# Kernel tuning notes

Hardware: AMD Instinct MI355X
Metric: run time of the kernel (lower is better)

## Reference

```python
import jax, jax.numpy as jnp
import numpy as np

B, N, D, H = 2, 2048, 384, 8
Dh = D // H          # 48
G = Dh // 3          # 16 3-vectors per head
EPS = 1e-5


def setup_inputs() -> dict:
    key = jax.random.key(0)
    ks = jax.random.split(key, 8)
    x = jax.random.normal(ks[0], (B, N, D), dtype=jnp.float32)
    # per-node SE(3) frames: proper rotation matrices via QR of random Gaussians
    raw = jax.random.normal(ks[1], (B, N, 3, 3), dtype=jnp.float32)
    q, r = jnp.linalg.qr(raw)
    sign = jnp.sign(jnp.diagonal(r, axis1=-2, axis2=-1))
    frames = q * sign[..., None, :]
    s = 1.0 / np.sqrt(D)
    Wq = jax.random.normal(ks[2], (D, D), dtype=jnp.float32) * s
    Wk = jax.random.normal(ks[3], (D, D), dtype=jnp.float32) * s
    Wv = jax.random.normal(ks[4], (D, D), dtype=jnp.float32) * s
    Wo = jax.random.normal(ks[5], (D, D), dtype=jnp.float32) * s
    bo = jnp.zeros((D,), dtype=jnp.float32)
    gamma = jnp.ones((D,), dtype=jnp.float32)
    beta = jnp.zeros((D,), dtype=jnp.float32)
    return {"x": x, "frames": frames, "Wq": Wq, "Wk": Wk, "Wv": Wv,
            "Wo": Wo, "bo": bo, "gamma": gamma, "beta": beta}


def _rotate(frames, t):
    # t: [B,N,H,Dh] -> rotate each 3-vector chunk by the node's frame R_i
    b, n, h, dh = t.shape
    t3 = t.reshape(b, n, h, dh // 3, 3)
    r3 = jnp.einsum('bnij,bnhgj->bnhgi', frames, t3)
    return r3.reshape(b, n, h, dh)


def reference(x, frames, Wq, Wk, Wv, Wo, bo, gamma, beta):
    b, n, d = x.shape
    Q = (x @ Wq.T).reshape(b, n, H, Dh)
    K = (x @ Wk.T).reshape(b, n, H, Dh)
    V = (x @ Wv.T).reshape(b, n, H, Dh)
    # SE(3) frame-conditioned attention: rotate Q,K into each node's local frame
    Qr = _rotate(frames, Q)
    Kr = _rotate(frames, K)
    scores = jnp.einsum('bqhd,bkhd->bhqk', Qr, Kr) / np.sqrt(Dh)
    attn = jax.nn.softmax(scores, axis=-1)
    out = jnp.einsum('bhqk,bkhd->bqhd', attn, V).reshape(b, n, d)
    out = out @ Wo.T + bo          # out_proj; dropout is identity in eval
    y = x + out                     # residual
    mu = jnp.mean(y, axis=-1, keepdims=True)
    var = jnp.var(y, axis=-1, keepdims=True)
    return (y - mu) * jax.lax.rsqrt(var + EPS) * gamma + beta
```

## Files before the change

kernel.cpp:

```cpp
#include <hip/hip_runtime.h>
#include <hip/hip_bf16.h>
#include <math.h>

constexpr int B = 2, N = 2048, D = 384, H = 8, Dh = 48;
constexpr int M = B * N;
constexpr float EPS = 1e-5f;
constexpr int WSZ = 384 * 384;

typedef short bf16x8 __attribute__((ext_vector_type(8)));
typedef float f32x4 __attribute__((ext_vector_type(4)));

#if __has_builtin(__builtin_amdgcn_exp2f)
#define EXP2(x) __builtin_amdgcn_exp2f(x)
#else
#define EXP2(x) exp2f(x)
#endif

__device__ __forceinline__ ushort f2bf(float f) {
  union { float f; uint u; } v; v.f = f;
  uint r = v.u + 0x7fffu + ((v.u >> 16) & 1u);
  return (ushort)(r >> 16);
}
__device__ __forceinline__ float bf2f(ushort u) {
  union { uint u; float f; } v; v.u = ((uint)u) << 16;
  return v.f;
}
__device__ __forceinline__ uint pk_bf16(float lo, float hi) {
  union { __hip_bfloat162 h; uint u; } v;
  v.h = __float22bfloat162_rn(make_float2(lo, hi));
  return v.u;
}

__device__ __forceinline__ void gload16(const void* g, void* lds) {
  __builtin_amdgcn_global_load_lds(
      (const __attribute__((address_space(1))) unsigned int*)g,
      (__attribute__((address_space(3))) unsigned int*)lds, 16, 0, 0);
}

__global__ __launch_bounds__(256) void pack_all(
    const float* __restrict__ x, const float* __restrict__ Wq,
    const float* __restrict__ Wk, const float* __restrict__ Wv,
    const float* __restrict__ Wo, ushort* __restrict__ xbf,
    ushort* __restrict__ Wqkv, ushort* __restrict__ Wobf) {
  constexpr int XSZ = M * 384;
  int i = (blockIdx.x * 256 + threadIdx.x) * 8;
  const float* src; ushort* dst; int off;
  if (i < XSZ) { src = x; dst = xbf; off = i; }
  else {
    int j = i - XSZ;
    if (j < WSZ)          { src = Wq; dst = Wqkv;           off = j; }
    else if (j < 2 * WSZ) { src = Wk; dst = Wqkv + WSZ;     off = j - WSZ; }
    else if (j < 3 * WSZ) { src = Wv; dst = Wqkv + 2 * WSZ; off = j - 2 * WSZ; }
    else                  { src = Wo; dst = Wobf;           off = j - 3 * WSZ; }
  }
  float4 a = *(const float4*)(src + off);
  float4 b = *(const float4*)(src + off + 4);
  uint4 o;
  o.x = pk_bf16(a.x, a.y);
  o.y = pk_bf16(a.z, a.w);
  o.z = pk_bf16(b.x, b.y);
  o.w = pk_bf16(b.z, b.w);
  *(uint4*)(dst + off) = o;
}

__global__ __launch_bounds__(256) void gemm_qkv(
    const ushort* __restrict__ Abf, const ushort* __restrict__ Wbf,
    ushort* __restrict__ Qpad, ushort* __restrict__ Kpad,
    ushort* __restrict__ Vt) {
  __shared__ ushort Asm[64 * 32];
  __shared__ ushort Bsm[128 * 32];
  const int tid = threadIdx.x, w = tid >> 6, lane = tid & 63;
  const int lq = lane & 15, g = lane >> 4;
  const int brow = blockIdx.y * 64, bcol = blockIdx.x * 128;
  const int wr0 = (w >> 1) * 32, wc0 = (w & 1) * 64;
  const int srow = lane >> 2, scol = (lane & 3) * 8;
  f32x4 acc[2][4];
#pragma unroll
  for (int mi = 0; mi < 2; ++mi)
#pragma unroll
    for (int ni = 0; ni < 4; ++ni) acc[mi][ni] = f32x4{0.f, 0.f, 0.f, 0.f};

  for (int kt = 0; kt < 384; kt += 32) {
    __syncthreads();
    gload16(Abf + (size_t)(brow + w * 16 + srow) * 384 + kt + scol, Asm + w * 512);
#pragma unroll
    for (int i = 0; i < 2; ++i) {
      int seg = w * 2 + i;
      gload16(Wbf + (size_t)(bcol + seg * 16 + srow) * 384 + kt + scol, Bsm + seg * 512);
    }
    __syncthreads();
    bf16x8 a[2], b[4];
#pragma unroll
    for (int mi = 0; mi < 2; ++mi)
      a[mi] = *(const bf16x8*)(Asm + (wr0 + mi * 16 + lq) * 32 + g * 8);
#pragma unroll
    for (int ni = 0; ni < 4; ++ni)
      b[ni] = *(const bf16x8*)(Bsm + (wc0 + ni * 16 + lq) * 32 + g * 8);
#pragma unroll
    for (int mi = 0; mi < 2; ++mi)
#pragma unroll
      for (int ni = 0; ni < 4; ++ni)
        acc[mi][ni] = __builtin_amdgcn_mfma_f32_16x16x32_bf16(a[mi], b[ni], acc[mi][ni], 0, 0, 0);
  }

  if (bcol < 768) {
#pragma unroll
    for (int mi = 0; mi < 2; ++mi)
#pragma unroll
      for (int ni = 0; ni < 4; ++ni) {
        int colD = bcol + wc0 + ni * 16 + lq;
        ushort* dstm = (colD < 384) ? Qpad : Kpad;
        int c = (colD < 384) ? colD : colD - 384;
        int hh = c / 48, dh = c - hh * 48;
#pragma unroll
        for (int r = 0; r < 4; ++r) {
          int row = brow + wr0 + mi * 16 + g * 4 + r;
          dstm[(size_t)row * 512 + hh * 64 + dh] = f2bf(acc[mi][ni][r]);
        }
      }
  } else {
#pragma unroll
    for (int mi = 0; mi < 2; ++mi)
#pragma unroll
      for (int ni = 0; ni < 4; ++ni) {
        int vcol = bcol + wc0 + ni * 16 + lq - 768;
        int hh = vcol / 48, dh = vcol - hh * 48;
#pragma unroll
        for (int r = 0; r < 4; ++r) {
          int row = brow + wr0 + mi * 16 + g * 4 + r;
          int bb = row >> 11, nn = row & 2047;
          Vt[((size_t)(bb * H + hh) * 48 + dh) * N + nn] = f2bf(acc[mi][ni][r]);
        }
      }
  }
}

__global__ __launch_bounds__(256) void rotate_both(
    ushort* __restrict__ Q, ushort* __restrict__ K,
    const float* __restrict__ F, float qscale) {
  int idx = blockIdx.x * 256 + threadIdx.x;
  int h = idx & 7;
  int bn = (idx >> 3) & 4095;
  int mat = idx >> 15;
  ushort* p = (mat ? K : Q) + (size_t)bn * 512 + h * 64;
  float scale = mat ? 1.0f : qscale;
  const float* R = F + (size_t)bn * 9;
  float r0 = R[0], r1 = R[1], r2 = R[2];
  float r3 = R[3], r4 = R[4], r5 = R[5];
  float r6 = R[6], r7 = R[7], r8 = R[8];
  uint u[24];
#pragma unroll
  for (int j = 0; j < 6; ++j)
    *(uint4*)(u + j * 4) = *(const uint4*)(p + j * 8);
  float f[48];
#pragma unroll
  for (int j = 0; j < 24; ++j) {
    f[2 * j] = bf2f((ushort)u[j]);
    f[2 * j + 1] = bf2f((ushort)(u[j] >> 16));
  }
  float o[48];
#pragma unroll
  for (int t = 0; t < 16; ++t) {
    float v0 = f[3 * t], v1 = f[3 * t + 1], v2 = f[3 * t + 2];
    o[3 * t]     = (r0 * v0 + r1 * v1 + r2 * v2) * scale;
    o[3 * t + 1] = (r3 * v0 + r4 * v1 + r5 * v2) * scale;
    o[3 * t + 2] = (r6 * v0 + r7 * v1 + r8 * v2) * scale;
  }
  uint ow[24];
#pragma unroll
  for (int j = 0; j < 24; ++j) ow[j] = pk_bf16(o[2 * j], o[2 * j + 1]);
#pragma unroll
  for (int j = 0; j < 6; ++j)
    *(uint4*)(p + j * 8) = *(uint4*)(ow + j * 4);
  uint4 z = make_uint4(0, 0, 0, 0);
  *(uint4*)(p + 48) = z;
  *(uint4*)(p + 56) = z;
}

__global__ __launch_bounds__(256) void attn_mfma(
    const ushort* __restrict__ Qpad, const ushort* __restrict__ Kpad,
    const ushort* __restrict__ Vt, ushort* __restrict__ Pacc,
    float* __restrict__ Pml) {
  __shared__ __align__(16) ushort SH[14336];
  ushort* K0 = SH;
  ushort* K1 = SH + 4096;
  ushort* V0 = SH + 8192;
  ushort* V1 = SH + 11264;

  const int bid = blockIdx.x;
  const int wg = (bid & 7) * 64 + (bid >> 3);
  const int qt = wg & 15;
  const int rest = wg >> 4;
  const int h = rest & 7;
  const int b = (rest >> 3) & 1;
  const int half = rest >> 4;
  const int kt0 = half * 1024;
  const int tid = threadIdx.x;
  const int w = tid >> 6;
  const int lane = tid & 63;
  const int lq = lane & 15;
  const int g = lane >> 4;
  const int l7 = lq & 7;
  const int srow8 = lane >> 3;
  const int c8 = (lane & 7) ^ srow8;

  bf16x8 qf[2][2];
  {
    const ushort* qb = Qpad + ((size_t)(b * N) + qt * 128 + w * 32) * 512 + h * 64;
#pragma unroll
    for (int i = 0; i < 2; ++i)
#pragma unroll
      for (int kd = 0; kd < 2; ++kd)
        qf[i][kd] = *(const bf16x8*)(qb + (size_t)(i * 16 + lq) * 512 + kd * 32 + g * 8);
  }

  const ushort* kg0;
  const ushort* kg1;
  {
    int s0 = w;
    int k0i = (s0 >> 2) * 32 + (s0 & 1) * 16 + (srow8 >> 2) * 8 + ((s0 >> 1) & 1) * 4 + (srow8 & 3);
    kg0 = Kpad + ((size_t)(b * N) + kt0 + k0i) * 512 + h * 64 + c8 * 8;
    int s1 = w + 4;
    int k1i = (s1 >> 2) * 32 + (s1 & 1) * 16 + (srow8 >> 2) * 8 + ((s1 >> 1) & 1) * 4 + (srow8 & 3);
    kg1 = Kpad + ((size_t)(b * N) + kt0 + k1i) * 512 + h * 64 + c8 * 8;
  }
  const ushort* vg0 = Vt + ((size_t)(b * H + h) * 48 + w * 8 + srow8) * (size_t)N + kt0 + c8 * 8;
  const ushort* vg1 = vg0 + 32 * (size_t)N;

  auto stage = [&](ushort* kb, ushort* vb) {
    gload16(kg0, kb + w * 512);
    gload16(kg1, kb + (w + 4) * 512);
    gload16(vg0, vb + w * 512);
    if (w < 2) gload16(vg1, vb + (w + 4) * 512);
    kg0 += 64 * 512; kg1 += 64 * 512; vg0 += 64; vg1 += 64;
  };

  float m[2] = {-3.0e38f, -3.0e38f}, l[2] = {0.f, 0.f};
  f32x4 oacc[2][3];
#pragma unroll
  for (int i = 0; i < 2; ++i)
#pragma unroll
    for (int d = 0; d < 3; ++d) oacc[i][d] = f32x4{0.f, 0.f, 0.f, 0.f};

  stage(K0, V0);
  __syncthreads();
  int cur = 0;

  for (int t = 0; t < 16; ++t) {
    if (t < 15) stage(cur ? K0 : K1, cur ? V0 : V1);
    const ushort* Kc = cur ? K1 : K0;
    const ushort* Vc = cur ? V1 : V0;

    f32x4 st[2][4];
#pragma unroll
    for (int i = 0; i < 2; ++i)
#pragma unroll
      for (int t4 = 0; t4 < 4; ++t4) st[i][t4] = f32x4{0.f, 0.f, 0.f, 0.f};
#pragma unroll
    for (int t4 = 0; t4 < 4; ++t4) {
      bf16x8 a0 = *(const bf16x8*)(Kc + (t4 * 16 + lq) * 64 + ((g ^ l7) * 8));
      bf16x8 a1 = *(const bf16x8*)(Kc + (t4 * 16 + lq) * 64 + (((g + 4) ^ l7) * 8));
#pragma unroll
      for (int i = 0; i < 2; ++i) {
        st[i][t4] = __builtin_amdgcn_mfma_f32_16x16x32_bf16(a0, qf[i][0], st[i][t4], 0, 0, 0);
        st[i][t4] = __builtin_amdgcn_mfma_f32_16x16x32_bf16(a1, qf[i][1], st[i][t4], 0, 0, 0);
      }
    }

    bf16x8 vf[2][3];
#pragma unroll
    for (int ks = 0; ks < 2; ++ks)
#pragma unroll
      for (int d = 0; d < 3; ++d)
        vf[ks][d] = *(const bf16x8*)(Vc + (d * 16 + lq) * 64 + ((((ks << 2) | g) ^ l7) * 8));

    float tmax[2];
#pragma unroll
    for (int i = 0; i < 2; ++i) {
      float t0 = st[i][0][0];
#pragma unroll
      for (int t4 = 0; t4 < 4; ++t4)
#pragma unroll
        for (int r = 0; r < 4; ++r) t0 = fmaxf(t0, st[i][t4][r]);
      t0 = fmaxf(t0, __shfl_xor(t0, 16));
      t0 = fmaxf(t0, __shfl_xor(t0, 32));
      tmax[i] = t0;
    }
    bool need = (tmax[0] > m[0] + 8.0f) | (tmax[1] > m[1] + 8.0f);
    if (__ballot(need)) {
#pragma unroll
      for (int i = 0; i < 2; ++i) {
        float mnew = fmaxf(m[i], tmax[i]);
        float corr = EXP2(m[i] - mnew);
        m[i] = mnew;
        l[i] *= corr;
#pragma unroll
        for (int r = 0; r < 4; ++r) {
          float cr = __shfl(corr, g * 4 + r);
#pragma unroll
          for (int d = 0; d < 3; ++d) oacc[i][d][r] *= cr;
        }
      }
    }

    bf16x8 pf[2][2];
#pragma unroll
    for (int i = 0; i < 2; ++i) {
      float ps = 0.f;
      uint u0[4], u1[4];
#pragma unroll
      for (int t4 = 0; t4 < 4; ++t4) {
        float p0 = EXP2(st[i][t4][0] - m[i]);
        float p1 = EXP2(st[i][t4][1] - m[i]);
        float p2 = EXP2(st[i][t4][2] - m[i]);
        float p3 = EXP2(st[i][t4][3] - m[i]);
        ps += (p0 + p1) + (p2 + p3);
        if (t4 < 2) {
          u0[(t4 & 1) * 2]     = pk_bf16(p0, p1);
          u0[(t4 & 1) * 2 + 1] = pk_bf16(p2, p3);
        } else {
          u1[(t4 & 1) * 2]     = pk_bf16(p0, p1);
          u1[(t4 & 1) * 2 + 1] = pk_bf16(p2, p3);
        }
      }
      ps += __shfl_xor(ps, 16);
      ps += __shfl_xor(ps, 32);
      l[i] += ps;
      union { uint4 q; bf16x8 v; } c0, c1;
      c0.q = make_uint4(u0[0], u0[1], u0[2], u0[3]);
      c1.q = make_uint4(u1[0], u1[1], u1[2], u1[3]);
      pf[i][0] = c0.v;
      pf[i][1] = c1.v;
    }

#pragma unroll
    for (int ks = 0; ks < 2; ++ks)
#pragma unroll
      for (int i = 0; i < 2; ++i)
#pragma unroll
        for (int d = 0; d < 3; ++d)
          oacc[i][d] = __builtin_amdgcn_mfma_f32_16x16x32_bf16(pf[i][ks], vf[ks][d], oacc[i][d], 0, 0, 0);

    __syncthreads();
    cur ^= 1;
  }

#pragma unroll
  for (int i = 0; i < 2; ++i) {
    const size_t pr0 = ((size_t)((half * B + b) * H + h)) * N + qt * 128 + w * 32 + i * 16;
#pragma unroll
    for (int d = 0; d < 3; ++d)
#pragma unroll
      for (int r = 0; r < 4; ++r)
        Pacc[(pr0 + g * 4 + r) * 48 + d * 16 + lq] = f2bf(oacc[i][d][r]);
    if (g == 0) {
      Pml[(pr0 + lq) * 2] = m[i];
      Pml[(pr0 + lq) * 2 + 1] = l[i];
    }
  }
}

__global__ __launch_bounds__(256) void gemm_out_ln(
    const ushort* __restrict__ Pacc, const float* __restrict__ Pml,
    const ushort* __restrict__ Wbf, const float* __restrict__ x,
    const float* __restrict__ bo, const float* __restrict__ gamma,
    const float* __restrict__ beta, float* __restrict__ out) {
  __shared__ ushort Asm[16 * 32];
  __shared__ ushort Bsm[384 * 32];
  __shared__ float red[4][16][2];
  __shared__ float Wm[16][8][2];
  const int tid = threadIdx.x, w = tid >> 6, lane = tid & 63;
  const int lq = lane & 15, g = lane >> 4;
  const int brow = blockIdx.x * 16;
  const int srow = lane >> 2, scol = (lane & 3) * 8;

  if (tid < 128) {
    int r = tid >> 3, hh = tid & 7;
    int gr = brow + r;
    int bb = gr >> 11, nn = gr & 2047;
    size_t i0 = ((size_t)(bb * H + hh)) * N + nn;
    size_t i1 = ((size_t)((B + bb) * H + hh)) * N + nn;
    float m0 = Pml[i0 * 2], l0 = Pml[i0 * 2 + 1];
    float m1 = Pml[i1 * 2], l1 = Pml[i1 * 2 + 1];
    float mm = fmaxf(m0, m1);
    float e0 = EXP2(m0 - mm), e1 = EXP2(m1 - mm);
    float inv = 1.f / (l0 * e0 + l1 * e1);
    Wm[r][hh][0] = e0 * inv;
    Wm[r][hh][1] = e1 * inv;
  }
  __syncthreads();

  f32x4 acc[6];
#pragma unroll
  for (int ni = 0; ni < 6; ++ni) acc[ni] = f32x4{0.f, 0.f, 0.f, 0.f};

  for (int kt = 0; kt < 384; kt += 32) {
    __syncthreads();
    if (w == 0) {
      int col = kt + scol;
      int hh = col / 48;
      int dcol = col - hh * 48;
      int gr = brow + srow;
      int bb = gr >> 11, nn = gr & 2047;
      const ushort* a0p = Pacc + (((size_t)(bb * H + hh)) * N + nn) * 48 + dcol;
      const ushort* a1p = Pacc + (((size_t)((B + bb) * H + hh)) * N + nn) * 48 + dcol;
      bf16x8 a0 = *(const bf16x8*)a0p;
      bf16x8 a1 = *(const bf16x8*)a1p;
      float w0v = Wm[srow][hh][0], w1v = Wm[srow][hh][1];
      uint mg[4];
#pragma unroll
      for (int j = 0; j < 4; ++j)
        mg[j] = pk_bf16(
            bf2f((ushort)a0[2 * j]) * w0v + bf2f((ushort)a1[2 * j]) * w1v,
            bf2f((ushort)a0[2 * j + 1]) * w0v + bf2f((ushort)a1[2 * j + 1]) * w1v);
      *(uint4*)(Asm + srow * 32 + scol) = make_uint4(mg[0], mg[1], mg[2], mg[3]);
    }
#pragma unroll
    for (int i = 0; i < 6; ++i) {
      int seg = w * 6 + i;
      gload16(Wbf + (size_t)(seg * 16 + srow) * 384 + kt + scol, Bsm + seg * 512);
    }
    __syncthreads();
    bf16x8 a = *(const bf16x8*)(Asm + lq * 32 + g * 8);
#pragma unroll
    for (int ni = 0; ni < 6; ++ni) {
      bf16x8 bb2 = *(const bf16x8*)(Bsm + ((w * 6 + ni) * 16 + lq) * 32 + g * 8);
      acc[ni] = __builtin_amdgcn_mfma_f32_16x16x32_bf16(a, bb2, acc[ni], 0, 0, 0);
    }
  }

  float s[4] = {0.f, 0.f, 0.f, 0.f}, s2[4] = {0.f, 0.f, 0.f, 0.f};
#pragma unroll
  for (int ni = 0; ni < 6; ++ni) {
    int col = (w * 6 + ni) * 16 + lq;
    float bcol = bo[col];
#pragma unroll
    for (int r = 0; r < 4; ++r) {
      float y = acc[ni][r] + x[(size_t)(brow + g * 4 + r) * 384 + col] + bcol;
      acc[ni][r] = y;
      s[r] += y; s2[r] += y * y;
    }
  }
#pragma unroll
  for (int o = 1; o < 16; o <<= 1) {
#pragma unroll
    for (int r = 0; r < 4; ++r) {
      s[r] += __shfl_xor(s[r], o);
      s2[r] += __shfl_xor(s2[r], o);
    }
  }
  if (lq == 0) {
#pragma unroll
    for (int r = 0; r < 4; ++r) {
      red[w][g * 4 + r][0] = s[r];
      red[w][g * 4 + r][1] = s2[r];
    }
  }
  __syncthreads();
#pragma unroll
  for (int r = 0; r < 4; ++r) {
    int row = g * 4 + r;
    float ts  = red[0][row][0] + red[1][row][0] + red[2][row][0] + red[3][row][0];
    float ts2 = red[0][row][1] + red[1][row][1] + red[2][row][1] + red[3][row][1];
    float mu = ts * (1.f / 384.f);
    float var = ts2 * (1.f / 384.f) - mu * mu;
    float rstd = rsqrtf(var + EPS);
    float* orow = out + (size_t)(brow + row) * 384;
#pragma unroll
    for (int ni = 0; ni < 6; ++ni) {
      int col = (w * 6 + ni) * 16 + lq;
      orow[col] = (acc[ni][r] - mu) * rstd * gamma[col] + beta[col];
    }
  }
}

extern "C" void kernel_launch(void* const* d_in, const int* in_sizes, int n_in,
                              void* d_out, int out_size, void* d_ws, size_t ws_size,
                              hipStream_t stream) {
  const float* x      = (const float*)d_in[0];
  const float* frames = (const float*)d_in[1];
  const float* Wq     = (const float*)d_in[2];
  const float* Wk     = (const float*)d_in[3];
  const float* Wv     = (const float*)d_in[4];
  const float* Wo     = (const float*)d_in[5];
  const float* bo     = (const float*)d_in[6];
  const float* gamma  = (const float*)d_in[7];
  const float* beta   = (const float*)d_in[8];
  float* out = (float*)d_out;

  ushort* xbf  = (ushort*)d_ws;
  ushort* Wqkv = xbf + (size_t)M * 384;
  ushort* Wobf = Wqkv + 3 * (size_t)WSZ;
  ushort* Qpad = Wobf + (size_t)WSZ;
  ushort* Kpad = Qpad + (size_t)M * 512;
  ushort* Vt   = Kpad + (size_t)M * 512;
  ushort* Pacc = Vt + (size_t)M * 384;
  float*  Pml  = (float*)(Pacc + (size_t)2 * B * H * N * 48);

  const float qscale = 0.14433756729740643f * 1.4426950408889634f;

  pack_all<<<(M * 384 + 4 * WSZ) / (8 * 256), 256, 0, stream>>>(
      x, Wq, Wk, Wv, Wo, xbf, Wqkv, Wobf);

  gemm_qkv<<<dim3(9, 64), 256, 0, stream>>>(xbf, Wqkv, Qpad, Kpad, Vt);

  rotate_both<<<2 * M * H / 256, 256, 0, stream>>>(Qpad, Kpad, frames, qscale);

  attn_mfma<<<2 * B * H * (N / 128), 256, 0, stream>>>(Qpad, Kpad, Vt, Pacc, Pml);

  gemm_out_ln<<<M / 16, 256, 0, stream>>>(Pacc, Pml, Wobf, x, bo, gamma, beta, out);
}
```

Before: 74.67 us.

## Split attention KV into four chunks and double-buffer GEMM tile loads

The attention kernel now splits the key/value range into four chunks instead of two. The grid grows to 1024 workgroups, which should fill more of the CUs, and the out-projection kernel merges four partial softmax results. Both GEMM kernels now double-buffer their shared-memory tile loads, so each k-step issues one barrier instead of two. The out-projection also builds the merged attention A-tile once up front, using all threads. The cost is more partial-output traffic and workspace, plus extra shared memory.

```diff
diff --git a/kernel.cpp b/kernel.cpp
--- a/kernel.cpp
+++ b/kernel.cpp
@@ -6,6 +6,7 @@
 constexpr int M = B * N;
 constexpr float EPS = 1e-5f;
 constexpr int WSZ = 384 * 384;
+constexpr int SPLIT = 4;
 
 typedef short bf16x8 __attribute__((ext_vector_type(8)));
 typedef float f32x4 __attribute__((ext_vector_type(4)));
@@ -67,40 +68,48 @@
     const ushort* __restrict__ Abf, const ushort* __restrict__ Wbf,
     ushort* __restrict__ Qpad, ushort* __restrict__ Kpad,
     ushort* __restrict__ Vt) {
-  __shared__ ushort Asm[64 * 32];
-  __shared__ ushort Bsm[128 * 32];
+  __shared__ ushort Asm[2][64 * 32];
+  __shared__ ushort Bsm[2][128 * 32];
   const int tid = threadIdx.x, w = tid >> 6, lane = tid & 63;
   const int lq = lane & 15, g = lane >> 4;
   const int brow = blockIdx.y * 64, bcol = blockIdx.x * 128;
   const int wr0 = (w >> 1) * 32, wc0 = (w & 1) * 64;
   const int srow = lane >> 2, scol = (lane & 3) * 8;
-  f32x4 acc[2][4];
-#pragma unroll
-  for (int mi = 0; mi < 2; ++mi)
-#pragma unroll
-    for (int ni = 0; ni < 4; ++ni) acc[mi][ni] = f32x4{0.f, 0.f, 0.f, 0.f};
-
-  for (int kt = 0; kt < 384; kt += 32) {
-    __syncthreads();
-    gload16(Abf + (size_t)(brow + w * 16 + srow) * 384 + kt + scol, Asm + w * 512);
+
+  auto stageQ = [&](int buf, int kt) {
+    gload16(Abf + (size_t)(brow + w * 16 + srow) * 384 + kt + scol, Asm[buf] + w * 512);
 #pragma unroll
     for (int i = 0; i < 2; ++i) {
       int seg = w * 2 + i;
-      gload16(Wbf + (size_t)(bcol + seg * 16 + srow) * 384 + kt + scol, Bsm + seg * 512);
-    }
-    __syncthreads();
+      gload16(Wbf + (size_t)(bcol + seg * 16 + srow) * 384 + kt + scol, Bsm[buf] + seg * 512);
+    }
+  };
+
+  f32x4 acc[2][4];
+#pragma unroll
+  for (int mi = 0; mi < 2; ++mi)
+#pragma unroll
+    for (int ni = 0; ni < 4; ++ni) acc[mi][ni] = f32x4{0.f, 0.f, 0.f, 0.f};
+
+  stageQ(0, 0);
+  __syncthreads();
+  for (int ki = 0; ki < 12; ++ki) {
+    if (ki < 11) stageQ((ki & 1) ^ 1, (ki + 1) * 32);
+    const ushort* Ac = Asm[ki & 1];
+    const ushort* Bc = Bsm[ki & 1];
     bf16x8 a[2], b[4];
 #pragma unroll
     for (int mi = 0; mi < 2; ++mi)
-      a[mi] = *(const bf16x8*)(Asm + (wr0 + mi * 16 + lq) * 32 + g * 8);
+      a[mi] = *(const bf16x8*)(Ac + (wr0 + mi * 16 + lq) * 32 + g * 8);
 #pragma unroll
     for (int ni = 0; ni < 4; ++ni)
-      b[ni] = *(const bf16x8*)(Bsm + (wc0 + ni * 16 + lq) * 32 + g * 8);
+      b[ni] = *(const bf16x8*)(Bc + (wc0 + ni * 16 + lq) * 32 + g * 8);
 #pragma unroll
     for (int mi = 0; mi < 2; ++mi)
 #pragma unroll
       for (int ni = 0; ni < 4; ++ni)
         acc[mi][ni] = __builtin_amdgcn_mfma_f32_16x16x32_bf16(a[mi], b[ni], acc[mi][ni], 0, 0, 0);
+    __syncthreads();
   }
 
   if (bcol < 768) {
@@ -188,13 +197,13 @@
   ushort* V1 = SH + 11264;
 
   const int bid = blockIdx.x;
-  const int wg = (bid & 7) * 64 + (bid >> 3);
+  const int wg = (bid & 7) * 128 + (bid >> 3);
   const int qt = wg & 15;
   const int rest = wg >> 4;
   const int h = rest & 7;
   const int b = (rest >> 3) & 1;
-  const int half = rest >> 4;
-  const int kt0 = half * 1024;
+  const int quarter = rest >> 4;
+  const int kt0 = quarter * (N / SPLIT);
   const int tid = threadIdx.x;
   const int w = tid >> 6;
   const int lane = tid & 63;
@@ -246,8 +255,8 @@
   __syncthreads();
   int cur = 0;
 
-  for (int t = 0; t < 16; ++t) {
-    if (t < 15) stage(cur ? K0 : K1, cur ? V0 : V1);
+  for (int t = 0; t < N / SPLIT / 64; ++t) {
+    if (t < N / SPLIT / 64 - 1) stage(cur ? K0 : K1, cur ? V0 : V1);
     const ushort* Kc = cur ? K1 : K0;
     const ushort* Vc = cur ? V1 : V0;
 
@@ -347,7 +356,7 @@
 
 #pragma unroll
   for (int i = 0; i < 2; ++i) {
-    const size_t pr0 = ((size_t)((half * B + b) * H + h)) * N + qt * 128 + w * 32 + i * 16;
+    const size_t pr0 = ((size_t)((quarter * B + b) * H + h)) * N + qt * 128 + w * 32 + i * 16;
 #pragma unroll
     for (int d = 0; d < 3; ++d)
 #pragma unroll
@@ -365,10 +374,10 @@
     const ushort* __restrict__ Wbf, const float* __restrict__ x,
     const float* __restrict__ bo, const float* __restrict__ gamma,
     const float* __restrict__ beta, float* __restrict__ out) {
-  __shared__ ushort Asm[16 * 32];
-  __shared__ ushort Bsm[384 * 32];
+  __shared__ ushort Asm[16 * 392];
+  __shared__ ushort Bsm[2][384 * 32];
   __shared__ float red[4][16][2];
-  __shared__ float Wm[16][8][2];
+  __shared__ float Wm[16][8][SPLIT];
   const int tid = threadIdx.x, w = tid >> 6, lane = tid & 63;
   const int lq = lane & 15, g = lane >> 4;
   const int brow = blockIdx.x * 16;
@@ -378,55 +387,73 @@
     int r = tid >> 3, hh = tid & 7;
     int gr = brow + r;
     int bb = gr >> 11, nn = gr & 2047;
-    size_t i0 = ((size_t)(bb * H + hh)) * N + nn;
-    size_t i1 = ((size_t)((B + bb) * H + hh)) * N + nn;
-    float m0 = Pml[i0 * 2], l0 = Pml[i0 * 2 + 1];
-    float m1 = Pml[i1 * 2], l1 = Pml[i1 * 2 + 1];
-    float mm = fmaxf(m0, m1);
-    float e0 = EXP2(m0 - mm), e1 = EXP2(m1 - mm);
-    float inv = 1.f / (l0 * e0 + l1 * e1);
-    Wm[r][hh][0] = e0 * inv;
-    Wm[r][hh][1] = e1 * inv;
+    float mq[SPLIT], lq4[SPLIT];
+    float mm = -3.0e38f;
+#pragma unroll
+    for (int s = 0; s < SPLIT; ++s) {
+      size_t is = ((size_t)((s * B + bb) * H + hh)) * N + nn;
+      mq[s] = Pml[is * 2]; lq4[s] = Pml[is * 2 + 1];
+      mm = fmaxf(mm, mq[s]);
+    }
+    float inv = 0.f, e[SPLIT];
+#pragma unroll
+    for (int s = 0; s < SPLIT; ++s) { e[s] = EXP2(mq[s] - mm); inv += lq4[s] * e[s]; }
+    inv = 1.f / inv;
+#pragma unroll
+    for (int s = 0; s < SPLIT; ++s) Wm[r][hh][s] = e[s] * inv;
   }
   __syncthreads();
 
-  f32x4 acc[6];
-#pragma unroll
-  for (int ni = 0; ni < 6; ++ni) acc[ni] = f32x4{0.f, 0.f, 0.f, 0.f};
-
-  for (int kt = 0; kt < 384; kt += 32) {
-    __syncthreads();
-    if (w == 0) {
-      int col = kt + scol;
-      int hh = col / 48;
-      int dcol = col - hh * 48;
-      int gr = brow + srow;
-      int bb = gr >> 11, nn = gr & 2047;
-      const ushort* a0p = Pacc + (((size_t)(bb * H + hh)) * N + nn) * 48 + dcol;
-      const ushort* a1p = Pacc + (((size_t)((B + bb) * H + hh)) * N + nn) * 48 + dcol;
-      bf16x8 a0 = *(const bf16x8*)a0p;
-      bf16x8 a1 = *(const bf16x8*)a1p;
-      float w0v = Wm[srow][hh][0], w1v = Wm[srow][hh][1];
-      uint mg[4];
-#pragma unroll
-      for (int j = 0; j < 4; ++j)
-        mg[j] = pk_bf16(
-            bf2f((ushort)a0[2 * j]) * w0v + bf2f((ushort)a1[2 * j]) * w1v,
-            bf2f((ushort)a0[2 * j + 1]) * w0v + bf2f((ushort)a1[2 * j + 1]) * w1v);
-      *(uint4*)(Asm + srow * 32 + scol) = make_uint4(mg[0], mg[1], mg[2], mg[3]);
-    }
+  auto stageB = [&](int buf, int kt) {
 #pragma unroll
     for (int i = 0; i < 6; ++i) {
       int seg = w * 6 + i;
-      gload16(Wbf + (size_t)(seg * 16 + srow) * 384 + kt + scol, Bsm + seg * 512);
+      gload16(Wbf + (size_t)(seg * 16 + srow) * 384 + kt + scol, Bsm[buf] + seg * 512);
+    }
+  };
+
+#pragma unroll
+  for (int it = 0; it < 3; ++it) {
+    int e8 = tid + it * 256;
+    int r = e8 / 48, cb = e8 - r * 48;
+    int col = cb * 8;
+    int hh = col / 48, dcol = col - hh * 48;
+    int gr = brow + r;
+    int bb = gr >> 11, nn = gr & 2047;
+    float a8[8] = {0.f, 0.f, 0.f, 0.f, 0.f, 0.f, 0.f, 0.f};
+#pragma unroll
+    for (int s = 0; s < SPLIT; ++s) {
+      const ushort* ps = Pacc + (((size_t)((s * B + bb) * H + hh)) * N + nn) * 48 + dcol;
+      bf16x8 v = *(const bf16x8*)ps;
+      float wv = Wm[r][hh][s];
+#pragma unroll
+      for (int j = 0; j < 8; ++j) a8[j] += bf2f((ushort)v[j]) * wv;
+    }
+    uint4 o;
+    o.x = pk_bf16(a8[0], a8[1]);
+    o.y = pk_bf16(a8[2], a8[3]);
+    o.z = pk_bf16(a8[4], a8[5]);
+    o.w = pk_bf16(a8[6], a8[7]);
+    *(uint4*)(Asm + r * 392 + col) = o;
+  }
+
+  stageB(0, 0);
+  __syncthreads();
+
+  f32x4 acc[6];
+#pragma unroll
+  for (int ni = 0; ni < 6; ++ni) acc[ni] = f32x4{0.f, 0.f, 0.f, 0.f};
+
+  for (int ki = 0; ki < 12; ++ki) {
+    if (ki < 11) stageB((ki & 1) ^ 1, (ki + 1) * 32);
+    const ushort* Bc = Bsm[ki & 1];
+    bf16x8 a = *(const bf16x8*)(Asm + lq * 392 + ki * 32 + g * 8);
+#pragma unroll
+    for (int ni = 0; ni < 6; ++ni) {
+      bf16x8 bb2 = *(const bf16x8*)(Bc + ((w * 6 + ni) * 16 + lq) * 32 + g * 8);
+      acc[ni] = __builtin_amdgcn_mfma_f32_16x16x32_bf16(a, bb2, acc[ni], 0, 0, 0);
     }
     __syncthreads();
-    bf16x8 a = *(const bf16x8*)(Asm + lq * 32 + g * 8);
-#pragma unroll
-    for (int ni = 0; ni < 6; ++ni) {
-      bf16x8 bb2 = *(const bf16x8*)(Bsm + ((w * 6 + ni) * 16 + lq) * 32 + g * 8);
-      acc[ni] = __builtin_amdgcn_mfma_f32_16x16x32_bf16(a, bb2, acc[ni], 0, 0, 0);
-    }
   }
 
   float s[4] = {0.f, 0.f, 0.f, 0.f}, s2[4] = {0.f, 0.f, 0.f, 0.f};
@@ -495,7 +522,7 @@
   ushort* Kpad = Qpad + (size_t)M * 512;
   ushort* Vt   = Kpad + (size_t)M * 512;
   ushort* Pacc = Vt + (size_t)M * 384;
-  float*  Pml  = (float*)(Pacc + (size_t)2 * B * H * N * 48);
+  float*  Pml  = (float*)(Pacc + (size_t)SPLIT * B * H * N * 48);
 
   const float qscale = 0.14433756729740643f * 1.4426950408889634f;
 
@@ -506,7 +533,7 @@
 
   rotate_both<<<2 * M * H / 256, 256, 0, stream>>>(Qpad, Kpad, frames, qscale);
 
-  attn_mfma<<<2 * B * H * (N / 128), 256, 0, stream>>>(Qpad, Kpad, Vt, Pacc, Pml);
+  attn_mfma<<<SPLIT * B * H * (N / 128), 256, 0, stream>>>(Qpad, Kpad, Vt, Pacc, Pml);
 
   gemm_out_ln<<<M / 16, 256, 0, stream>>>(Pacc, Pml, Wobf, x, bo, gamma, beta, out);
 }
```

After: 76.16 us. No clear change (+2.0%).
